# Optimization experiments

Measured on AMD Instinct MI355X. Metric: run time of the kernel, lower is better.

Reference implementation:

```python
import jax, jax.numpy as jnp
import numpy as np

H = 256       # hidden_size
W2V = 300     # word embedding dim
POS = 30      # pos embedding dim
NF = 100      # filters per n-gram CNN
VOCAB = 50000
NPOS = 100
N_EDUS = 1024
L = 20        # tokens per EDU


def setup_inputs() -> dict:
    key = jax.random.key(0)
    ks = jax.random.split(key, 22)
    def nrm(k, shape, s=0.05):
        return jax.random.normal(k, shape, dtype=jnp.float32) * s
    cw = W2V + POS  # CNN input width = 330
    # valid transition sequence: S, then (S, R) repeated n-1 times -> 2n-1 steps
    transes = jnp.concatenate([jnp.zeros((1,), jnp.int32),
                               jnp.tile(jnp.array([0, 1], jnp.int32), N_EDUS - 1)])
    return {
        "edu_words": jax.random.randint(ks[0], (N_EDUS, L), 0, VOCAB),
        "edu_poses": jax.random.randint(ks[1], (N_EDUS, L), 0, NPOS),
        "transes": transes,
        "word_emb": nrm(ks[2], (VOCAB, W2V), 1.0),
        "pos_emb": nrm(ks[3], (NPOS, POS), 1.0),
        "Wu": nrm(ks[4], (NF, 1, 1, cw)), "bu": nrm(ks[5], (NF,)),
        "Wb": nrm(ks[6], (NF, 1, 2, cw)), "bb": nrm(ks[7], (NF,)),
        "Wt": nrm(ks[8], (NF, 1, 3, cw)), "bt": nrm(ks[9], (NF,)),
        "Wp": nrm(ks[10], (2 * H, 2 * W2V + POS + 3 * NF)), "bp": nrm(ks[11], (2 * H,)),
        "Wih": nrm(ks[12], (4 * H, 3 * H)), "Whh": nrm(ks[13], (4 * H, H)),
        "bih": nrm(ks[14], (4 * H,)), "bhh": nrm(ks[15], (4 * H,)),
        "Wc": nrm(ks[16], (5 * H, 3 * H)), "bc": nrm(ks[17], (5 * H,)),
        "Ws": nrm(ks[18], (2, H)), "bs": nrm(ks[19], (2,)),
    }


def _encode_edus(edu_words, edu_poses, word_emb, pos_emb, Wu, bu, Wb, bb, Wt, bt, Wp, bp):
    we = word_emb[edu_words]                # [N, L, 300]
    pe = pos_emb[edu_poses]                 # [N, L, 30]
    x = jnp.concatenate([we, pe], axis=-1)[:, None, :, :]  # NCHW [N,1,L,330]
    def conv_pool(W, b, pad):
        # kernel spans full width -> output width 1; pad only along time
        y = jax.lax.conv_general_dilated(x, W, (1, 1), ((pad, pad), (0, 0)),
                                         dimension_numbers=("NCHW", "OIHW", "NCHW"))[..., 0]
        return jax.nn.relu(y + b[None, :, None]).max(axis=-1)  # [N, F]
    feats = jnp.concatenate([we[:, 0], we[:, -1], pe[:, 0],
                             conv_pool(Wu, bu, 0), conv_pool(Wb, bb, 1),
                             conv_pool(Wt, bt, 2)], axis=-1)   # [N, 930]
    h, c = jnp.split(feats @ Wp.T + bp, 2, axis=-1)
    return h, c


def _parse_loss(edu_words, edu_poses, transes, word_emb, pos_emb, Wu, bu, Wb, bb, Wt, bt,
                Wp, bp, Wih, Whh, bih, bhh, Wc, bc, Ws, bs):
    eh, ec = _encode_edus(edu_words, edu_poses, word_emb, pos_emb, Wu, bu, Wb, bb, Wt, bt, Wp, bp)
    M = N_EDUS + 2
    buf_h = jnp.concatenate([eh, jnp.zeros((2, H), jnp.float32)], axis=0)
    buf_c = jnp.concatenate([ec, jnp.zeros((2, H), jnp.float32)], axis=0)
    stack_h = jnp.zeros((M, H), jnp.float32)  # slots 0,1 are the initial placeholders
    stack_c = jnp.zeros((M, H), jnp.float32)

    def lstm(xv, h, c):  # torch LSTMCell gate order i,f,g,o
        g = xv @ Wih.T + bih + h @ Whh.T + bhh
        i, f, gg, o = jnp.split(g, 4)
        c2 = jax.nn.sigmoid(f) * c + jax.nn.sigmoid(i) * jnp.tanh(gg)
        return jax.nn.sigmoid(o) * jnp.tanh(c2), c2

    def track(sh, sptr, bptr, th, tc):
        xv = jnp.concatenate([sh[sptr - 1], sh[sptr - 2], buf_h[bptr]])
        return lstm(xv, th, tc)

    sptr = jnp.int32(2)
    bptr = jnp.int32(0)
    th, tc = track(stack_h, sptr, bptr, jnp.zeros(H, jnp.float32), jnp.zeros(H, jnp.float32))

    def step(carry, trans):
        sh, sc, sptr, bptr, th, tc = carry
        logits = th @ Ws.T + bs  # scorer MLP with mlp_layers=1 -> single Linear
        is_shift = trans == 0
        # SHIFT candidate: push buffer front
        sh_s = sh.at[sptr].set(buf_h[bptr])
        sc_s = sc.at[sptr].set(buf_c[bptr])
        # REDUCE candidate: tree-LSTM composition of top two stack items
        h1, c1 = sh[sptr - 1], sc[sptr - 1]
        h2, c2 = sh[sptr - 2], sc[sptr - 2]
        g = jnp.concatenate([h1, h2, th]) @ Wc.T + bc
        a, i, f1, f2, o = jnp.split(g, 5)
        rc = jnp.tanh(a) * jax.nn.sigmoid(i) + jax.nn.sigmoid(f1) * c1 + jax.nn.sigmoid(f2) * c2
        rh = jax.nn.sigmoid(o) * jnp.tanh(rc)
        sh_r = sh.at[sptr - 2].set(rh)
        sc_r = sc.at[sptr - 2].set(rc)
        sh2 = jnp.where(is_shift, sh_s, sh_r)
        sc2 = jnp.where(is_shift, sc_s, sc_r)
        sptr2 = jnp.where(is_shift, sptr + 1, sptr - 1)
        bptr2 = jnp.where(is_shift, bptr + 1, bptr)
        th2, tc2 = track(sh2, sptr2, bptr2, th, tc)
        return (sh2, sc2, sptr2, bptr2, th2, tc2), logits

    _, pred = jax.lax.scan(step, (stack_h, stack_c, sptr, bptr, th, tc), transes)
    logp = jax.nn.log_softmax(pred, axis=-1)
    return -jnp.mean(logp[jnp.arange(transes.shape[0]), transes])


def reference(edu_words, edu_poses, transes, word_emb, pos_emb, Wu, bu, Wb, bb, Wt, bt,
              Wp, bp, Wih, Whh, bih, bhh, Wc, bc, Ws, bs):
    return _parse_loss(edu_words, edu_poses, transes, word_emb, pos_emb, Wu, bu, Wb, bb,
                       Wt, bt, Wp, bp, Wih, Whh, bih, bhh, Wc, bc, Ws, bs)
```

## Files before the change

### kernel.cpp

```cpp
#include <hip/hip_runtime.h>
#include <math.h>

#define NEDU  1024
#define LTOK  20
#define CW    330
#define HDIM  256
#define FEAT  930
#define MSLOT 1026
#define NWG   64

#define O_WCATT 0
#define SZ_WCATT (330*600)
#define O_F     (O_WCATT + SZ_WCATT)
#define SZ_F    (NEDU*FEAT)
#define O_BUFH  (O_F + SZ_F)
#define SZ_BUF  (MSLOT*HDIM)
#define O_BUFC  (O_BUFH + SZ_BUF)
#define O_STKT  (O_BUFC + SZ_BUF)
#define O_THT   (O_STKT + MSLOT*HDIM)
#define O_RHT   (O_THT + 2*HDIM)
#define O_LOSSP (O_RHT + HDIM)
#define NZERO   ((MSLOT + 3) * HDIM)

#define AG __HIP_MEMORY_SCOPE_AGENT
__device__ __forceinline__ unsigned long long aload64(const unsigned long long* p) {
  return __hip_atomic_load(p, __ATOMIC_RELAXED, AG);
}
__device__ __forceinline__ void astore(unsigned* p, unsigned v) {
  __hip_atomic_store(p, v, __ATOMIC_RELAXED, AG);
}
__device__ __forceinline__ unsigned tagbits(float v, unsigned ver) {
  return (__float_as_uint(v) & ~3u) | (ver & 3u);
}
__device__ __forceinline__ float sigm(float x) { return 1.f / (1.f + expf(-x)); }

__device__ __forceinline__ void sync_lds() {
  asm volatile("s_waitcnt lgkmcnt(0)\n\ts_barrier" ::: "memory");
}

__device__ __forceinline__ void gather1T(const unsigned* base, int lane, unsigned tag,
                                         float* x) {
  const unsigned long long* p = (const unsigned long long*)base + 2 * lane;
  for (int it = 0;; ++it) {
    const unsigned long long a = aload64(p), b = aload64(p + 1);
    const bool ok = (((unsigned)a & 3u) == tag) & (((unsigned)(a >> 32) & 3u) == tag) &
                    (((unsigned)b & 3u) == tag) & (((unsigned)(b >> 32) & 3u) == tag);
    if (__ballot(ok) == ~0ull) {
      x[0] = __uint_as_float((unsigned)a); x[1] = __uint_as_float((unsigned)(a >> 32));
      x[2] = __uint_as_float((unsigned)b); x[3] = __uint_as_float((unsigned)(b >> 32));
      return;
    }
    if (it > 48) __builtin_amdgcn_s_sleep(1);
  }
}
__device__ __forceinline__ void gather2T(const unsigned* b1, unsigned t1,
                                         const unsigned* b2, unsigned t2,
                                         int lane, float* x1, float* x2) {
  const unsigned long long* p1 = (const unsigned long long*)b1 + 2 * lane;
  const unsigned long long* p2 = (const unsigned long long*)b2 + 2 * lane;
  for (int it = 0;; ++it) {
    const unsigned long long a = aload64(p1), b = aload64(p1 + 1);
    const unsigned long long c = aload64(p2), d = aload64(p2 + 1);
    const bool ok = (((unsigned)a & 3u) == t1) & (((unsigned)(a >> 32) & 3u) == t1) &
                    (((unsigned)b & 3u) == t1) & (((unsigned)(b >> 32) & 3u) == t1) &
                    (((unsigned)c & 3u) == t2) & (((unsigned)(c >> 32) & 3u) == t2) &
                    (((unsigned)d & 3u) == t2) & (((unsigned)(d >> 32) & 3u) == t2);
    if (__ballot(ok) == ~0ull) {
      x1[0] = __uint_as_float((unsigned)a); x1[1] = __uint_as_float((unsigned)(a >> 32));
      x1[2] = __uint_as_float((unsigned)b); x1[3] = __uint_as_float((unsigned)(b >> 32));
      x2[0] = __uint_as_float((unsigned)c); x2[1] = __uint_as_float((unsigned)(c >> 32));
      x2[2] = __uint_as_float((unsigned)d); x2[3] = __uint_as_float((unsigned)(d >> 32));
      return;
    }
    if (it > 48) __builtin_amdgcn_s_sleep(1);
  }
}

__global__ void prep_kernel(const float* __restrict__ Wu, const float* __restrict__ Wb,
                            const float* __restrict__ Wt, float* __restrict__ ws) {
  const int i0 = blockIdx.x * blockDim.x + threadIdx.x;
  const int st = gridDim.x * blockDim.x;
  for (int i = i0; i < SZ_WCATT; i += st) {
    const int k = i / 600, c = i - 600 * k;
    float v;
    if (c < 100)      v = Wu[c * 330 + k];
    else if (c < 300) { const int q = c - 100; v = Wb[(q % 100) * 660 + (q / 100) * 330 + k]; }
    else              { const int q = c - 300; v = Wt[(q % 100) * 990 + (q / 100) * 330 + k]; }
    ws[O_WCATT + i] = v;
  }
  unsigned* z = (unsigned*)ws + O_STKT;
  for (int i = i0; i < NZERO; i += st) z[i] = 0u;
  for (int i = i0; i < 2 * HDIM; i += st) {
    ws[O_BUFH + NEDU * HDIM + i] = 0.f;
    ws[O_BUFC + NEDU * HDIM + i] = 0.f;
  }
}

__global__ __launch_bounds__(256) void encode_kernel(
    const int* __restrict__ edu_words, const int* __restrict__ edu_poses,
    const float* __restrict__ word_emb, const float* __restrict__ pos_emb,
    const float* __restrict__ bu, const float* __restrict__ bb,
    const float* __restrict__ bt, float* __restrict__ ws) {
  __shared__ __align__(16) float xlT[CW * LTOK];
  __shared__ float zl[300 * 21];
  __shared__ float convout[300];
  const int n = blockIdx.x, tid = threadIdx.x;
  const float* WcatT = ws + O_WCATT;

  for (int i = tid; i < LTOK * CW; i += 256) {
    const int l = i / CW, k = i - l * CW;
    float v;
    if (k < 300) v = word_emb[(size_t)edu_words[n * LTOK + l] * 300 + k];
    else         v = pos_emb[(size_t)edu_poses[n * LTOK + l] * 30 + (k - 300)];
    xlT[k * LTOK + l] = v;
  }
  __syncthreads();

  for (int f = tid; f < 300; f += 256) {
    float acc[LTOK];
#pragma unroll
    for (int l = 0; l < LTOK; ++l) acc[l] = 0.f;
    for (int k = 0; k < CW; ++k) {
      const float w = WcatT[k * 600 + f];
      const float4* xp = (const float4*)(xlT + k * LTOK);
      union { float4 v[5]; float s[20]; } xu;
      xu.v[0] = xp[0]; xu.v[1] = xp[1]; xu.v[2] = xp[2]; xu.v[3] = xp[3]; xu.v[4] = xp[4];
#pragma unroll
      for (int l = 0; l < LTOK; ++l) acc[l] += w * xu.s[l];
    }
#pragma unroll
    for (int l = 0; l < LTOK; ++l) zl[f * 21 + l] = acc[l];
  }
  __syncthreads();
  if (tid < 200) {
    float m;
    if (tid < 100) {
      const int f = tid; const float b = bu[f];
      m = zl[f * 21] + b;
      for (int l = 1; l < 20; ++l) m = fmaxf(m, zl[f * 21 + l] + b);
    } else {
      const int f = tid - 100; const float b = bb[f];
      const float* z0 = zl + (100 + f) * 21;
      const float* z1 = zl + (200 + f) * 21;
      m = z1[0] + b;
      for (int u = 1; u <= 19; ++u) m = fmaxf(m, z0[u - 1] + z1[u] + b);
      m = fmaxf(m, z0[19] + b);
    }
    convout[tid] = fmaxf(m, 0.f);
  }
  __syncthreads();

  for (int f = tid; f < 300; f += 256) {
    float acc[LTOK];
#pragma unroll
    for (int l = 0; l < LTOK; ++l) acc[l] = 0.f;
    for (int k = 0; k < CW; ++k) {
      const float w = WcatT[k * 600 + 300 + f];
      const float4* xp = (const float4*)(xlT + k * LTOK);
      union { float4 v[5]; float s[20]; } xu;
      xu.v[0] = xp[0]; xu.v[1] = xp[1]; xu.v[2] = xp[2]; xu.v[3] = xp[3]; xu.v[4] = xp[4];
#pragma unroll
      for (int l = 0; l < LTOK; ++l) acc[l] += w * xu.s[l];
    }
#pragma unroll
    for (int l = 0; l < LTOK; ++l) zl[f * 21 + l] = acc[l];
  }
  __syncthreads();
  if (tid < 100) {
    const int f = tid; const float b = bt[f];
    const float* z0 = zl + f * 21;
    const float* z1 = zl + (100 + f) * 21;
    const float* z2 = zl + (200 + f) * 21;
    float m = z2[0] + b;
    m = fmaxf(m, z1[0] + z2[1] + b);
    for (int u = 2; u <= 19; ++u) m = fmaxf(m, z0[u - 2] + z1[u - 1] + z2[u] + b);
    m = fmaxf(m, z0[18] + z1[19] + b);
    m = fmaxf(m, z0[19] + b);
    convout[200 + f] = fmaxf(m, 0.f);
  }
  __syncthreads();

  float* Fr = ws + O_F + (size_t)n * FEAT;
  for (int j = tid; j < FEAT; j += 256) {
    float v;
    if (j < 300)      v = xlT[j * LTOK + 0];
    else if (j < 600) v = xlT[(j - 300) * LTOK + 19];
    else if (j < 630) v = xlT[(j - 300) * LTOK + 0];
    else              v = convout[j - 630];
    Fr[j] = v;
  }
}

__global__ __launch_bounds__(256) void proj_kernel(const float* __restrict__ Wp,
                                                   const float* __restrict__ bp,
                                                   float* __restrict__ ws) {
  __shared__ float As[64][17];
  __shared__ float Bs[64][17];
  const float* F = ws + O_F;
  float* bufh = ws + O_BUFH;
  float* bufc = ws + O_BUFC;
  const int tid = threadIdx.x;
  const int m0 = blockIdx.x * 64, n0 = blockIdx.y * 64;
  const int mm0 = (tid & 15) * 4, nn0 = (tid >> 4) * 4;
  float acc[4][4] = {{0.f}};
  for (int k0 = 0; k0 < FEAT; k0 += 16) {
    for (int i = tid; i < 64 * 16; i += 256) {
      const int mm = i >> 4, kk = i & 15;
      const int gk = k0 + kk;
      As[mm][kk] = (gk < FEAT) ? F[(size_t)(m0 + mm) * FEAT + gk] : 0.f;
      Bs[mm][kk] = (gk < FEAT) ? Wp[(size_t)(n0 + mm) * FEAT + gk] : 0.f;
    }
    __syncthreads();
#pragma unroll
    for (int kk = 0; kk < 16; ++kk) {
      float av[4], bv[4];
#pragma unroll
      for (int i = 0; i < 4; ++i) av[i] = As[mm0 + i][kk];
#pragma unroll
      for (int j = 0; j < 4; ++j) bv[j] = Bs[nn0 + j][kk];
#pragma unroll
      for (int i = 0; i < 4; ++i)
#pragma unroll
        for (int j = 0; j < 4; ++j) acc[i][j] += av[i] * bv[j];
    }
    __syncthreads();
  }
#pragma unroll
  for (int i = 0; i < 4; ++i) {
    const int m = m0 + mm0 + i;
#pragma unroll
    for (int j = 0; j < 4; ++j) {
      const int nn = n0 + nn0 + j;
      const float v = acc[i][j] + bp[nn];
      if (nn < 256) bufh[(size_t)m * 256 + nn] = v;
      else          bufc[(size_t)m * 256 + (nn - 256)] = v;
    }
  }
}

__global__ __launch_bounds__(256, 1) void parse_kernel(
    const int* __restrict__ transes, int nT,
    const float* __restrict__ Wih, const float* __restrict__ Whh,
    const float* __restrict__ bih, const float* __restrict__ bhh,
    const float* __restrict__ Wc, const float* __restrict__ bc,
    const float* __restrict__ Wsc, float* __restrict__ ws) {
  const int tid = threadIdx.x;
  const int lane = tid & 63;
  const int wv = tid >> 6;
  const int bx = blockIdx.x;
  const int j0 = bx * 4;

  const float* bufh = ws + O_BUFH;
  const float* bufc = ws + O_BUFC;
  unsigned* stkT = (unsigned*)ws + O_STKT;
  unsigned* thT  = (unsigned*)ws + O_THT;
  unsigned* rhT  = (unsigned*)ws + O_RHT;
  float* lossp   = ws + O_LOSSP;

  __shared__ float sc_lds[MSLOT][4];
  __shared__ unsigned vstk[MSLOT];
  __shared__ float tc_lds[2][4];
  __shared__ float g_lds[20];
  __shared__ float rh_st[4];
  __shared__ float part_lds[8];

  float wt[4][16]; float bt_[4];
#pragma unroll
  for (int q = 0; q < 4; ++q) {
    const int rg = wv * 256 + j0 + q;
#pragma unroll
    for (int blk = 0; blk < 3; ++blk) {
      const float4 w = *(const float4*)(Wih + (size_t)rg * 768 + blk * 256 + 4 * lane);
      wt[q][4 * blk + 0] = w.x; wt[q][4 * blk + 1] = w.y;
      wt[q][4 * blk + 2] = w.z; wt[q][4 * blk + 3] = w.w;
    }
    const float4 wh = *(const float4*)(Whh + (size_t)rg * 256 + 4 * lane);
    wt[q][12] = wh.x; wt[q][13] = wh.y; wt[q][14] = wh.z; wt[q][15] = wh.w;
    bt_[q] = bih[rg] + bhh[rg];
  }
  float wcm[5][12]; float bc_[5];
#pragma unroll
  for (int q = 0; q < 5; ++q) {
    const int row = 5 * wv + q, gate = row >> 2, jj = row & 3;
    const int rg = gate * 256 + j0 + jj;
#pragma unroll
    for (int blk = 0; blk < 3; ++blk) {
      const float4 w = *(const float4*)(Wc + (size_t)rg * 768 + blk * 256 + 4 * lane);
      wcm[q][4 * blk + 0] = w.x; wcm[q][4 * blk + 1] = w.y;
      wcm[q][4 * blk + 2] = w.z; wcm[q][4 * blk + 3] = w.w;
    }
    bc_[q] = bc[rg];
  }
  float ws0 = 0.f, ws1 = 0.f;
  if (tid < 4) { ws0 = Wsc[j0 + tid]; ws1 = Wsc[256 + j0 + tid]; }

  for (int i = tid; i < MSLOT; i += 256) vstk[i] = 0u;
  if (tid < 4) { sc_lds[0][tid] = 0.f; sc_lds[1][tid] = 0.f;
                 tc_lds[0][tid] = 0.f; tc_lds[1][tid] = 0.f; }
  __syncthreads();

  unsigned V = 0, vrh = 0;
  int sptr = 2, bptr = 0;

  auto red4 = [&](float& a0, float& a1, float& a2, float& a3) {
#pragma unroll
    for (int off = 32; off; off >>= 1) {
      a0 += __shfl_down(a0, off, 64); a1 += __shfl_down(a1, off, 64);
      a2 += __shfl_down(a2, off, 64); a3 += __shfl_down(a3, off, 64);
    }
  };
  auto red5 = [&](float& a0, float& a1, float& a2, float& a3, float& a4) {
#pragma unroll
    for (int off = 32; off; off >>= 1) {
      a0 += __shfl_down(a0, off, 64); a1 += __shfl_down(a1, off, 64);
      a2 += __shfl_down(a2, off, 64); a3 += __shfl_down(a3, off, 64);
      a4 += __shfl_down(a4, off, 64);
    }
  };

  auto fin_track = [&]() {
    const int j = j0 + tid;
    const float gi = g_lds[tid], gf = g_lds[4 + tid], gg = g_lds[8 + tid], go = g_lds[12 + tid];
    const float cn = sigm(gf) * tc_lds[V & 1][tid] + sigm(gi) * tanhf(gg);
    tc_lds[(V + 1) & 1][tid] = cn;
    const float th = sigm(go) * tanhf(cn);
    astore(thT + ((V + 1) & 1) * HDIM + j, tagbits(th, V + 1));
    part_lds[tid] = ws0 * th; part_lds[4 + tid] = ws1 * th;
  };
  auto emit_loss = [&]() {
    float* lp = lossp + (size_t)V * 128 + bx * 2;
    lp[0] = part_lds[0] + part_lds[1] + part_lds[2] + part_lds[3];
    lp[1] = part_lds[4] + part_lds[5] + part_lds[6] + part_lds[7];
  };
  auto dyn_track = [&](const unsigned* fbase, unsigned ftag, int fblk,
                       float s0, float s1, float s2, float s3) {
    float x[4];
    gather1T(fbase, lane, ftag, x);
    float d0 = 0.f, d1 = 0.f, d2 = 0.f, d3 = 0.f;
#pragma unroll
    for (int c = 0; c < 4; ++c) {
      d0 += wt[0][4 * fblk + c] * x[c]; d1 += wt[1][4 * fblk + c] * x[c];
      d2 += wt[2][4 * fblk + c] * x[c]; d3 += wt[3][4 * fblk + c] * x[c];
    }
    red4(d0, d1, d2, d3);
    if (lane == 0) {
      g_lds[wv * 4 + 0] = s0 + d0 + bt_[0]; g_lds[wv * 4 + 1] = s1 + d1 + bt_[1];
      g_lds[wv * 4 + 2] = s2 + d2 + bt_[2]; g_lds[wv * 4 + 3] = s3 + d3 + bt_[3];
    }
    sync_lds();
    if (tid < 4) fin_track();
    if (tid == 0) emit_loss();
  };

  {
    float p1[4], p2[4];
    gather2T(stkT + HDIM, 0u, stkT, 0u, lane, p1, p2);
    const float4 f3 = *(const float4*)(bufh + 4 * lane);
    const float p3[4] = { f3.x, f3.y, f3.z, f3.w };
    float s0 = 0.f, s1 = 0.f, s2 = 0.f, s3 = 0.f;
#pragma unroll
    for (int c = 0; c < 4; ++c) {
      s0 += wt[0][c] * p1[c] + wt[0][4 + c] * p2[c] + wt[0][8 + c] * p3[c];
      s1 += wt[1][c] * p1[c] + wt[1][4 + c] * p2[c] + wt[1][8 + c] * p3[c];
      s2 += wt[2][c] * p1[c] + wt[2][4 + c] * p2[c] + wt[2][8 + c] * p3[c];
      s3 += wt[3][c] * p1[c] + wt[3][4 + c] * p2[c] + wt[3][8 + c] * p3[c];
    }
    red4(s0, s1, s2, s3);
    dyn_track(thT + (V & 1) * HDIM, V & 3, 3, s0, s1, s2, s3);
    sync_lds();
    V += 1;
  }

  for (int t = 0; t < nT; ++t) {
    const int tr = transes[t];
    if (tr) {
      {
        float h1[4], h2[4];
        gather2T(stkT + (size_t)(sptr - 1) * HDIM, vstk[sptr - 1] & 3,
                 stkT + (size_t)(sptr - 2) * HDIM, vstk[sptr - 2] & 3, lane, h1, h2);
        float s0 = 0.f, s1 = 0.f, s2 = 0.f, s3 = 0.f, s4 = 0.f;
#pragma unroll
        for (int c = 0; c < 4; ++c) {
          s0 += wcm[0][c] * h1[c] + wcm[0][4 + c] * h2[c];
          s1 += wcm[1][c] * h1[c] + wcm[1][4 + c] * h2[c];
          s2 += wcm[2][c] * h1[c] + wcm[2][4 + c] * h2[c];
          s3 += wcm[3][c] * h1[c] + wcm[3][4 + c] * h2[c];
          s4 += wcm[4][c] * h1[c] + wcm[4][4 + c] * h2[c];
        }
        red5(s0, s1, s2, s3, s4);
        float x[4];
        gather1T(thT + (V & 1) * HDIM, lane, V & 3, x);
        float d0 = 0.f, d1 = 0.f, d2 = 0.f, d3 = 0.f, d4 = 0.f;
#pragma unroll
        for (int c = 0; c < 4; ++c) {
          d0 += wcm[0][8 + c] * x[c]; d1 += wcm[1][8 + c] * x[c];
          d2 += wcm[2][8 + c] * x[c]; d3 += wcm[3][8 + c] * x[c];
          d4 += wcm[4][8 + c] * x[c];
        }
        red5(d0, d1, d2, d3, d4);
        if (lane == 0) {
          g_lds[5 * wv + 0] = s0 + d0 + bc_[0]; g_lds[5 * wv + 1] = s1 + d1 + bc_[1];
          g_lds[5 * wv + 2] = s2 + d2 + bc_[2]; g_lds[5 * wv + 3] = s3 + d3 + bc_[3];
          g_lds[5 * wv + 4] = s4 + d4 + bc_[4];
        }
      }
      sync_lds();
      if (tid < 4) {
        const int j = j0 + tid;
        const float ga = g_lds[tid], gi = g_lds[4 + tid], gf1 = g_lds[8 + tid],
                    gf2 = g_lds[12 + tid], go = g_lds[16 + tid];
        const float c1 = sc_lds[sptr - 1][tid];
        const float c2 = sc_lds[sptr - 2][tid];
        const float rc = tanhf(ga) * sigm(gi) + sigm(gf1) * c1 + sigm(gf2) * c2;
        const float rh = sigm(go) * tanhf(rc);
        sc_lds[sptr - 2][tid] = rc;
        rh_st[tid] = rh;
        astore(rhT + j, tagbits(rh, vrh + 1));
      }
      sync_lds();
      vrh += 1;

      {
        const int slot = sptr - 2;
        const unsigned nv = vstk[slot] + 1;
        if (tid < 4)
          astore(stkT + (size_t)slot * HDIM + j0 + tid, tagbits(rh_st[tid], nv));
        float p2[4], xth[4];
        gather2T(stkT + (size_t)(sptr - 3) * HDIM, vstk[sptr - 3] & 3,
                 thT + (V & 1) * HDIM, V & 3, lane, p2, xth);
        const float4 f3 = *(const float4*)(bufh + (size_t)bptr * HDIM + 4 * lane);
        const float p3[4] = { f3.x, f3.y, f3.z, f3.w };
        float s0 = 0.f, s1 = 0.f, s2 = 0.f, s3 = 0.f;
#pragma unroll
        for (int c = 0; c < 4; ++c) {
          s0 += wt[0][4 + c] * p2[c] + wt[0][8 + c] * p3[c] + wt[0][12 + c] * xth[c];
          s1 += wt[1][4 + c] * p2[c] + wt[1][8 + c] * p3[c] + wt[1][12 + c] * xth[c];
          s2 += wt[2][4 + c] * p2[c] + wt[2][8 + c] * p3[c] + wt[2][12 + c] * xth[c];
          s3 += wt[3][4 + c] * p2[c] + wt[3][8 + c] * p3[c] + wt[3][12 + c] * xth[c];
        }
        red4(s0, s1, s2, s3);
        dyn_track(rhT, vrh & 3, 0, s0, s1, s2, s3);
        if (tid == 0) vstk[slot] = nv;
        sync_lds();
        V += 1; sptr -= 1;
      }
    } else {
      const unsigned nv = vstk[sptr] + 1;
      if (tid < 4) {
        const int j = j0 + tid;
        astore(stkT + (size_t)sptr * HDIM + j, tagbits(bufh[(size_t)bptr * HDIM + j], nv));
        sc_lds[sptr][tid] = bufc[(size_t)bptr * HDIM + j];
      }
      const float4 f1 = *(const float4*)(bufh + (size_t)bptr * HDIM + 4 * lane);
      const float4 f3 = *(const float4*)(bufh + (size_t)(bptr + 1) * HDIM + 4 * lane);
      float p2[4];
      gather1T(stkT + (size_t)(sptr - 1) * HDIM, lane, vstk[sptr - 1] & 3, p2);
      const float p1[4] = { f1.x, f1.y, f1.z, f1.w };
      const float p3[4] = { f3.x, f3.y, f3.z, f3.w };
      float s0 = 0.f, s1 = 0.f, s2 = 0.f, s3 = 0.f;
#pragma unroll
      for (int c = 0; c < 4; ++c) {
        s0 += wt[0][c] * p1[c] + wt[0][4 + c] * p2[c] + wt[0][8 + c] * p3[c];
        s1 += wt[1][c] * p1[c] + wt[1][4 + c] * p2[c] + wt[1][8 + c] * p3[c];
        s2 += wt[2][c] * p1[c] + wt[2][4 + c] * p2[c] + wt[2][8 + c] * p3[c];
        s3 += wt[3][c] * p1[c] + wt[3][4 + c] * p2[c] + wt[3][8 + c] * p3[c];
      }
      red4(s0, s1, s2, s3);
      dyn_track(thT + (V & 1) * HDIM, V & 3, 3, s0, s1, s2, s3);
      if (tid == 0) vstk[sptr] = nv;
      sync_lds();
      V += 1; sptr += 1; bptr += 1;
    }
  }
}

__global__ __launch_bounds__(256) void loss_kernel(const int* __restrict__ transes, int nT,
                                                   const float* __restrict__ bsc,
                                                   const float* __restrict__ ws,
                                                   float* __restrict__ out) {
  const int tid = threadIdx.x;
  const float* lossp = ws + O_LOSSP;
  __shared__ double red[256];
  double acc = 0.0;
  for (int t = tid; t < nT; t += 256) {
    const float* lp = lossp + (size_t)t * 128;
    float a0 = 0.f, a1 = 0.f;
    for (int w = 0; w < 64; ++w) { a0 += lp[2 * w]; a1 += lp[2 * w + 1]; }
    const float l0 = a0 + bsc[0], l1 = a1 + bsc[1];
    const float mx = fmaxf(l0, l1);
    acc += (double)(mx + logf(expf(l0 - mx) + expf(l1 - mx)) - (transes[t] ? l1 : l0));
  }
  red[tid] = acc;
  __syncthreads();
  for (int s = 128; s; s >>= 1) {
    if (tid < s) red[tid] += red[tid + s];
    __syncthreads();
  }
  if (tid == 0) out[0] = (float)(red[0] / (double)nT);
}

extern "C" void kernel_launch(void* const* d_in, const int* in_sizes, int n_in,
                              void* d_out, int out_size, void* d_ws, size_t ws_size,
                              hipStream_t stream) {
  const int*   edu_words = (const int*)d_in[0];
  const int*   edu_poses = (const int*)d_in[1];
  const int*   transes   = (const int*)d_in[2];
  const float* word_emb  = (const float*)d_in[3];
  const float* pos_emb   = (const float*)d_in[4];
  const float* Wu  = (const float*)d_in[5];
  const float* bu  = (const float*)d_in[6];
  const float* Wb  = (const float*)d_in[7];
  const float* bb  = (const float*)d_in[8];
  const float* Wt  = (const float*)d_in[9];
  const float* bt  = (const float*)d_in[10];
  const float* Wp  = (const float*)d_in[11];
  const float* bp  = (const float*)d_in[12];
  const float* Wih = (const float*)d_in[13];
  const float* Whh = (const float*)d_in[14];
  const float* bih = (const float*)d_in[15];
  const float* bhh = (const float*)d_in[16];
  const float* Wc  = (const float*)d_in[17];
  const float* bc  = (const float*)d_in[18];
  const float* Wsc = (const float*)d_in[19];
  const float* bsc = (const float*)d_in[20];
  float* ws  = (float*)d_ws;
  float* out = (float*)d_out;
  int nT = in_sizes[2];

  hipLaunchKernelGGL(prep_kernel, dim3(256), dim3(256), 0, stream, Wu, Wb, Wt, ws);
  hipLaunchKernelGGL(encode_kernel, dim3(NEDU), dim3(256), 0, stream,
                     edu_words, edu_poses, word_emb, pos_emb, bu, bb, bt, ws);
  hipLaunchKernelGGL(proj_kernel, dim3(16, 8), dim3(256), 0, stream, Wp, bp, ws);

  void* args[] = { (void*)&transes, (void*)&nT, (void*)&Wih, (void*)&Whh, (void*)&bih,
                   (void*)&bhh, (void*)&Wc, (void*)&bc, (void*)&Wsc, (void*)&ws };
  hipLaunchCooperativeKernel((const void*)parse_kernel, dim3(NWG), dim3(256), args, 0, stream);

  hipLaunchKernelGGL(loss_kernel, dim3(1), dim3(256), 0, stream, transes, nT, bsc, ws, out);
}
```

Measured before the change: 7.783 ms.

## Restructure parse recurrence to one wavefront per hidden unit with double-buffered stack

The parse kernel now runs 256 single-wavefront workgroups, each owning one hidden unit, instead of 64 four-wave workgroups owning four units. All intra-block LDS barriers and shared gate staging are removed, and gate sums are reduced with xor butterflies so every lane holds the result. The stack is double-buffered by version parity so a reduce step's new value can be published and consumed without a separate rh buffer. Tracker-state loads are issued early and polled afterwards to overlap latency. Transitions are cached in LDS and the loss reduction is split into a parallel two-stage kernel. The tradeoff is four times as many cross-workgroup flag polls per step, and the loss-partial buffer now reuses the start of the workspace that the encoder weights occupied.

Result: slower. 13.26 ms (+70.4%).

```diff
diff --git a/kernel.cpp b/kernel.cpp
--- a/kernel.cpp
+++ b/kernel.cpp
@@ -7,23 +7,25 @@
 #define HDIM  256
 #define FEAT  930
 #define MSLOT 1026
-#define NWG   64
 
 #define O_WCATT 0
 #define SZ_WCATT (330*600)
 #define O_F     (O_WCATT + SZ_WCATT)
 #define SZ_F    (NEDU*FEAT)
+#define O_LOSSP 0
+#define SZ_LOSSP (2048*512)
 #define O_BUFH  (O_F + SZ_F)
 #define SZ_BUF  (MSLOT*HDIM)
 #define O_BUFC  (O_BUFH + SZ_BUF)
 #define O_STKT  (O_BUFC + SZ_BUF)
-#define O_THT   (O_STKT + MSLOT*HDIM)
-#define O_RHT   (O_THT + 2*HDIM)
-#define O_LOSSP (O_RHT + HDIM)
-#define NZERO   ((MSLOT + 3) * HDIM)
+#define O_THT   (O_STKT + 2*SZ_BUF)
+#define O_PART  (O_THT + 2*HDIM)
+#define NZERO   ((2*MSLOT + 2) * HDIM)
+
+typedef unsigned long long u64;
 
 #define AG __HIP_MEMORY_SCOPE_AGENT
-__device__ __forceinline__ unsigned long long aload64(const unsigned long long* p) {
+__device__ __forceinline__ u64 aload64(const u64* p) {
   return __hip_atomic_load(p, __ATOMIC_RELAXED, AG);
 }
 __device__ __forceinline__ void astore(unsigned* p, unsigned v) {
@@ -34,15 +36,11 @@
 }
 __device__ __forceinline__ float sigm(float x) { return 1.f / (1.f + expf(-x)); }
 
-__device__ __forceinline__ void sync_lds() {
-  asm volatile("s_waitcnt lgkmcnt(0)\n\ts_barrier" ::: "memory");
-}
-
 __device__ __forceinline__ void gather1T(const unsigned* base, int lane, unsigned tag,
                                          float* x) {
-  const unsigned long long* p = (const unsigned long long*)base + 2 * lane;
+  const u64* p = (const u64*)base + 2 * lane;
   for (int it = 0;; ++it) {
-    const unsigned long long a = aload64(p), b = aload64(p + 1);
+    const u64 a = aload64(p), b = aload64(p + 1);
     const bool ok = (((unsigned)a & 3u) == tag) & (((unsigned)(a >> 32) & 3u) == tag) &
                     (((unsigned)b & 3u) == tag) & (((unsigned)(b >> 32) & 3u) == tag);
     if (__ballot(ok) == ~0ull) {
@@ -56,11 +54,11 @@
 __device__ __forceinline__ void gather2T(const unsigned* b1, unsigned t1,
                                          const unsigned* b2, unsigned t2,
                                          int lane, float* x1, float* x2) {
-  const unsigned long long* p1 = (const unsigned long long*)b1 + 2 * lane;
-  const unsigned long long* p2 = (const unsigned long long*)b2 + 2 * lane;
+  const u64* p1 = (const u64*)b1 + 2 * lane;
+  const u64* p2 = (const u64*)b2 + 2 * lane;
   for (int it = 0;; ++it) {
-    const unsigned long long a = aload64(p1), b = aload64(p1 + 1);
-    const unsigned long long c = aload64(p2), d = aload64(p2 + 1);
+    const u64 a = aload64(p1), b = aload64(p1 + 1);
+    const u64 c = aload64(p2), d = aload64(p2 + 1);
     const bool ok = (((unsigned)a & 3u) == t1) & (((unsigned)(a >> 32) & 3u) == t1) &
                     (((unsigned)b & 3u) == t1) & (((unsigned)(b >> 32) & 3u) == t1) &
                     (((unsigned)c & 3u) == t2) & (((unsigned)(c >> 32) & 3u) == t2) &
@@ -74,6 +72,17 @@
     }
     if (it > 48) __builtin_amdgcn_s_sleep(1);
   }
+}
+__device__ __forceinline__ void spin4(const u64* p, u64 a, u64 b, unsigned tag, float* x) {
+  for (int it = 0;; ++it) {
+    const bool ok = (((unsigned)a & 3u) == tag) & (((unsigned)(a >> 32) & 3u) == tag) &
+                    (((unsigned)b & 3u) == tag) & (((unsigned)(b >> 32) & 3u) == tag);
+    if (__ballot(ok) == ~0ull) break;
+    if (it > 40) __builtin_amdgcn_s_sleep(1);
+    a = aload64(p); b = aload64(p + 1);
+  }
+  x[0] = __uint_as_float((unsigned)a); x[1] = __uint_as_float((unsigned)(a >> 32));
+  x[2] = __uint_as_float((unsigned)b); x[3] = __uint_as_float((unsigned)(b >> 32));
 }
 
 __global__ void prep_kernel(const float* __restrict__ Wu, const float* __restrict__ Wb,
@@ -217,11 +226,11 @@
 #pragma unroll
       for (int i = 0; i < 4; ++i) av[i] = As[mm0 + i][kk];
 #pragma unroll
-      for (int j = 0; j < 4; ++j) bv[j] = Bs[nn0 + j][kk];
+      for (int jj = 0; jj < 4; ++jj) bv[jj] = Bs[nn0 + jj][kk];
 #pragma unroll
       for (int i = 0; i < 4; ++i)
 #pragma unroll
-        for (int j = 0; j < 4; ++j) acc[i][j] += av[i] * bv[j];
+        for (int jj = 0; jj < 4; ++jj) acc[i][jj] += av[i] * bv[jj];
     }
     __syncthreads();
   }
@@ -229,274 +238,255 @@
   for (int i = 0; i < 4; ++i) {
     const int m = m0 + mm0 + i;
 #pragma unroll
-    for (int j = 0; j < 4; ++j) {
-      const int nn = n0 + nn0 + j;
-      const float v = acc[i][j] + bp[nn];
+    for (int jj = 0; jj < 4; ++jj) {
+      const int nn = n0 + nn0 + jj;
+      const float v = acc[i][jj] + bp[nn];
       if (nn < 256) bufh[(size_t)m * 256 + nn] = v;
       else          bufc[(size_t)m * 256 + (nn - 256)] = v;
     }
   }
 }
 
-__global__ __launch_bounds__(256, 1) void parse_kernel(
+__global__ __launch_bounds__(64, 1) void parse_kernel(
     const int* __restrict__ transes, int nT,
     const float* __restrict__ Wih, const float* __restrict__ Whh,
     const float* __restrict__ bih, const float* __restrict__ bhh,
     const float* __restrict__ Wc, const float* __restrict__ bc,
     const float* __restrict__ Wsc, float* __restrict__ ws) {
-  const int tid = threadIdx.x;
-  const int lane = tid & 63;
-  const int wv = tid >> 6;
-  const int bx = blockIdx.x;
-  const int j0 = bx * 4;
+  const int lane = threadIdx.x;
+  const int j = blockIdx.x;
 
   const float* bufh = ws + O_BUFH;
   const float* bufc = ws + O_BUFC;
   unsigned* stkT = (unsigned*)ws + O_STKT;
   unsigned* thT  = (unsigned*)ws + O_THT;
-  unsigned* rhT  = (unsigned*)ws + O_RHT;
   float* lossp   = ws + O_LOSSP;
 
-  __shared__ float sc_lds[MSLOT][4];
   __shared__ unsigned vstk[MSLOT];
-  __shared__ float tc_lds[2][4];
-  __shared__ float g_lds[20];
-  __shared__ float rh_st[4];
-  __shared__ float part_lds[8];
-
-  float wt[4][16]; float bt_[4];
-#pragma unroll
-  for (int q = 0; q < 4; ++q) {
-    const int rg = wv * 256 + j0 + q;
+  __shared__ float    scs[MSLOT];
+  __shared__ int      trs[2048];
+
+  for (int i = lane; i < MSLOT; i += 64) { vstk[i] = 0u; scs[i] = 0.f; }
+  const int nTc = (nT < 2048) ? nT : 2048;
+  for (int i = lane; i < nTc; i += 64) trs[i] = transes[i];
+  __syncthreads();
+
+  float wt[4][16]; float bt4[4];
+#pragma unroll
+  for (int g = 0; g < 4; ++g) {
+    const int rg = g * 256 + j;
 #pragma unroll
     for (int blk = 0; blk < 3; ++blk) {
       const float4 w = *(const float4*)(Wih + (size_t)rg * 768 + blk * 256 + 4 * lane);
-      wt[q][4 * blk + 0] = w.x; wt[q][4 * blk + 1] = w.y;
-      wt[q][4 * blk + 2] = w.z; wt[q][4 * blk + 3] = w.w;
+      wt[g][4 * blk + 0] = w.x; wt[g][4 * blk + 1] = w.y;
+      wt[g][4 * blk + 2] = w.z; wt[g][4 * blk + 3] = w.w;
     }
     const float4 wh = *(const float4*)(Whh + (size_t)rg * 256 + 4 * lane);
-    wt[q][12] = wh.x; wt[q][13] = wh.y; wt[q][14] = wh.z; wt[q][15] = wh.w;
-    bt_[q] = bih[rg] + bhh[rg];
-  }
-  float wcm[5][12]; float bc_[5];
+    wt[g][12] = wh.x; wt[g][13] = wh.y; wt[g][14] = wh.z; wt[g][15] = wh.w;
+    bt4[g] = bih[rg] + bhh[rg];
+  }
+  float wcm[5][12]; float bc5[5];
 #pragma unroll
   for (int q = 0; q < 5; ++q) {
-    const int row = 5 * wv + q, gate = row >> 2, jj = row & 3;
-    const int rg = gate * 256 + j0 + jj;
+    const int rg = q * 256 + j;
 #pragma unroll
     for (int blk = 0; blk < 3; ++blk) {
       const float4 w = *(const float4*)(Wc + (size_t)rg * 768 + blk * 256 + 4 * lane);
       wcm[q][4 * blk + 0] = w.x; wcm[q][4 * blk + 1] = w.y;
       wcm[q][4 * blk + 2] = w.z; wcm[q][4 * blk + 3] = w.w;
     }
-    bc_[q] = bc[rg];
-  }
-  float ws0 = 0.f, ws1 = 0.f;
-  if (tid < 4) { ws0 = Wsc[j0 + tid]; ws1 = Wsc[256 + j0 + tid]; }
-
-  for (int i = tid; i < MSLOT; i += 256) vstk[i] = 0u;
-  if (tid < 4) { sc_lds[0][tid] = 0.f; sc_lds[1][tid] = 0.f;
-                 tc_lds[0][tid] = 0.f; tc_lds[1][tid] = 0.f; }
-  __syncthreads();
-
-  unsigned V = 0, vrh = 0;
+    bc5[q] = bc[rg];
+  }
+  const float ws0 = Wsc[j], ws1 = Wsc[256 + j];
+
+  float tc = 0.f;
+  unsigned V = 0;
   int sptr = 2, bptr = 0;
 
-  auto red4 = [&](float& a0, float& a1, float& a2, float& a3) {
+  auto bfly4 = [&](float& a0, float& a1, float& a2, float& a3) {
 #pragma unroll
     for (int off = 32; off; off >>= 1) {
-      a0 += __shfl_down(a0, off, 64); a1 += __shfl_down(a1, off, 64);
-      a2 += __shfl_down(a2, off, 64); a3 += __shfl_down(a3, off, 64);
+      a0 += __shfl_xor(a0, off, 64); a1 += __shfl_xor(a1, off, 64);
+      a2 += __shfl_xor(a2, off, 64); a3 += __shfl_xor(a3, off, 64);
     }
   };
-  auto red5 = [&](float& a0, float& a1, float& a2, float& a3, float& a4) {
+  auto bfly5 = [&](float& a0, float& a1, float& a2, float& a3, float& a4) {
 #pragma unroll
     for (int off = 32; off; off >>= 1) {
-      a0 += __shfl_down(a0, off, 64); a1 += __shfl_down(a1, off, 64);
-      a2 += __shfl_down(a2, off, 64); a3 += __shfl_down(a3, off, 64);
-      a4 += __shfl_down(a4, off, 64);
+      a0 += __shfl_xor(a0, off, 64); a1 += __shfl_xor(a1, off, 64);
+      a2 += __shfl_xor(a2, off, 64); a3 += __shfl_xor(a3, off, 64);
+      a4 += __shfl_xor(a4, off, 64);
     }
   };
 
-  auto fin_track = [&]() {
-    const int j = j0 + tid;
-    const float gi = g_lds[tid], gf = g_lds[4 + tid], gg = g_lds[8 + tid], go = g_lds[12 + tid];
-    const float cn = sigm(gf) * tc_lds[V & 1][tid] + sigm(gi) * tanhf(gg);
-    tc_lds[(V + 1) & 1][tid] = cn;
+  auto fin_track = [&](float s0, float s1, float s2, float s3) {
+    const float gi = s0 + bt4[0], gf = s1 + bt4[1], gg = s2 + bt4[2], go = s3 + bt4[3];
+    const float cn = sigm(gf) * tc + sigm(gi) * tanhf(gg);
+    tc = cn;
     const float th = sigm(go) * tanhf(cn);
-    astore(thT + ((V + 1) & 1) * HDIM + j, tagbits(th, V + 1));
-    part_lds[tid] = ws0 * th; part_lds[4 + tid] = ws1 * th;
+    if (lane == 0) {
+      astore(thT + ((V + 1) & 1) * HDIM + j, tagbits(th, V + 1));
+      float2 lp; lp.x = ws0 * th; lp.y = ws1 * th;
+      *(float2*)(lossp + (size_t)V * 512 + 2 * j) = lp;
+    }
   };
-  auto emit_loss = [&]() {
-    float* lp = lossp + (size_t)V * 128 + bx * 2;
-    lp[0] = part_lds[0] + part_lds[1] + part_lds[2] + part_lds[3];
-    lp[1] = part_lds[4] + part_lds[5] + part_lds[6] + part_lds[7];
-  };
-  auto dyn_track = [&](const unsigned* fbase, unsigned ftag, int fblk,
-                       float s0, float s1, float s2, float s3) {
-    float x[4];
-    gather1T(fbase, lane, ftag, x);
-    float d0 = 0.f, d1 = 0.f, d2 = 0.f, d3 = 0.f;
+
+  {
+    const float4 f3 = *(const float4*)(bufh + 4 * lane);
+    const float x3[4] = { f3.x, f3.y, f3.z, f3.w };
+    float s0 = 0.f, s1 = 0.f, s2 = 0.f, s3 = 0.f;
 #pragma unroll
     for (int c = 0; c < 4; ++c) {
-      d0 += wt[0][4 * fblk + c] * x[c]; d1 += wt[1][4 * fblk + c] * x[c];
-      d2 += wt[2][4 * fblk + c] * x[c]; d3 += wt[3][4 * fblk + c] * x[c];
-    }
-    red4(d0, d1, d2, d3);
-    if (lane == 0) {
-      g_lds[wv * 4 + 0] = s0 + d0 + bt_[0]; g_lds[wv * 4 + 1] = s1 + d1 + bt_[1];
-      g_lds[wv * 4 + 2] = s2 + d2 + bt_[2]; g_lds[wv * 4 + 3] = s3 + d3 + bt_[3];
-    }
-    sync_lds();
-    if (tid < 4) fin_track();
-    if (tid == 0) emit_loss();
-  };
-
-  {
-    float p1[4], p2[4];
-    gather2T(stkT + HDIM, 0u, stkT, 0u, lane, p1, p2);
-    const float4 f3 = *(const float4*)(bufh + 4 * lane);
-    const float p3[4] = { f3.x, f3.y, f3.z, f3.w };
-    float s0 = 0.f, s1 = 0.f, s2 = 0.f, s3 = 0.f;
-#pragma unroll
-    for (int c = 0; c < 4; ++c) {
-      s0 += wt[0][c] * p1[c] + wt[0][4 + c] * p2[c] + wt[0][8 + c] * p3[c];
-      s1 += wt[1][c] * p1[c] + wt[1][4 + c] * p2[c] + wt[1][8 + c] * p3[c];
-      s2 += wt[2][c] * p1[c] + wt[2][4 + c] * p2[c] + wt[2][8 + c] * p3[c];
-      s3 += wt[3][c] * p1[c] + wt[3][4 + c] * p2[c] + wt[3][8 + c] * p3[c];
-    }
-    red4(s0, s1, s2, s3);
-    dyn_track(thT + (V & 1) * HDIM, V & 3, 3, s0, s1, s2, s3);
-    sync_lds();
-    V += 1;
+      s0 += wt[0][8 + c] * x3[c]; s1 += wt[1][8 + c] * x3[c];
+      s2 += wt[2][8 + c] * x3[c]; s3 += wt[3][8 + c] * x3[c];
+    }
+    bfly4(s0, s1, s2, s3);
+    fin_track(s0, s1, s2, s3);
+    V = 1;
   }
 
   for (int t = 0; t < nT; ++t) {
-    const int tr = transes[t];
+    const int tr = (t < 2048) ? trs[t] : transes[t];
+    const u64* pt = (const u64*)(thT + (V & 1) * HDIM) + 2 * lane;
+    u64 ta = aload64(pt), tb = aload64(pt + 1);
     if (tr) {
-      {
-        float h1[4], h2[4];
-        gather2T(stkT + (size_t)(sptr - 1) * HDIM, vstk[sptr - 1] & 3,
-                 stkT + (size_t)(sptr - 2) * HDIM, vstk[sptr - 2] & 3, lane, h1, h2);
-        float s0 = 0.f, s1 = 0.f, s2 = 0.f, s3 = 0.f, s4 = 0.f;
-#pragma unroll
-        for (int c = 0; c < 4; ++c) {
-          s0 += wcm[0][c] * h1[c] + wcm[0][4 + c] * h2[c];
-          s1 += wcm[1][c] * h1[c] + wcm[1][4 + c] * h2[c];
-          s2 += wcm[2][c] * h1[c] + wcm[2][4 + c] * h2[c];
-          s3 += wcm[3][c] * h1[c] + wcm[3][4 + c] * h2[c];
-          s4 += wcm[4][c] * h1[c] + wcm[4][4 + c] * h2[c];
-        }
-        red5(s0, s1, s2, s3, s4);
-        float x[4];
-        gather1T(thT + (V & 1) * HDIM, lane, V & 3, x);
-        float d0 = 0.f, d1 = 0.f, d2 = 0.f, d3 = 0.f, d4 = 0.f;
-#pragma unroll
-        for (int c = 0; c < 4; ++c) {
-          d0 += wcm[0][8 + c] * x[c]; d1 += wcm[1][8 + c] * x[c];
-          d2 += wcm[2][8 + c] * x[c]; d3 += wcm[3][8 + c] * x[c];
-          d4 += wcm[4][8 + c] * x[c];
-        }
-        red5(d0, d1, d2, d3, d4);
-        if (lane == 0) {
-          g_lds[5 * wv + 0] = s0 + d0 + bc_[0]; g_lds[5 * wv + 1] = s1 + d1 + bc_[1];
-          g_lds[5 * wv + 2] = s2 + d2 + bc_[2]; g_lds[5 * wv + 3] = s3 + d3 + bc_[3];
-          g_lds[5 * wv + 4] = s4 + d4 + bc_[4];
-        }
-      }
-      sync_lds();
-      if (tid < 4) {
-        const int j = j0 + tid;
-        const float ga = g_lds[tid], gi = g_lds[4 + tid], gf1 = g_lds[8 + tid],
-                    gf2 = g_lds[12 + tid], go = g_lds[16 + tid];
-        const float c1 = sc_lds[sptr - 1][tid];
-        const float c2 = sc_lds[sptr - 2][tid];
-        const float rc = tanhf(ga) * sigm(gi) + sigm(gf1) * c1 + sigm(gf2) * c2;
-        const float rh = sigm(go) * tanhf(rc);
-        sc_lds[sptr - 2][tid] = rc;
-        rh_st[tid] = rh;
-        astore(rhT + j, tagbits(rh, vrh + 1));
-      }
-      sync_lds();
-      vrh += 1;
-
-      {
-        const int slot = sptr - 2;
-        const unsigned nv = vstk[slot] + 1;
-        if (tid < 4)
-          astore(stkT + (size_t)slot * HDIM + j0 + tid, tagbits(rh_st[tid], nv));
-        float p2[4], xth[4];
-        gather2T(stkT + (size_t)(sptr - 3) * HDIM, vstk[sptr - 3] & 3,
-                 thT + (V & 1) * HDIM, V & 3, lane, p2, xth);
-        const float4 f3 = *(const float4*)(bufh + (size_t)bptr * HDIM + 4 * lane);
-        const float p3[4] = { f3.x, f3.y, f3.z, f3.w };
-        float s0 = 0.f, s1 = 0.f, s2 = 0.f, s3 = 0.f;
-#pragma unroll
-        for (int c = 0; c < 4; ++c) {
-          s0 += wt[0][4 + c] * p2[c] + wt[0][8 + c] * p3[c] + wt[0][12 + c] * xth[c];
-          s1 += wt[1][4 + c] * p2[c] + wt[1][8 + c] * p3[c] + wt[1][12 + c] * xth[c];
-          s2 += wt[2][4 + c] * p2[c] + wt[2][8 + c] * p3[c] + wt[2][12 + c] * xth[c];
-          s3 += wt[3][4 + c] * p2[c] + wt[3][8 + c] * p3[c] + wt[3][12 + c] * xth[c];
-        }
-        red4(s0, s1, s2, s3);
-        dyn_track(rhT, vrh & 3, 0, s0, s1, s2, s3);
-        if (tid == 0) vstk[slot] = nv;
-        sync_lds();
-        V += 1; sptr -= 1;
-      }
+      const unsigned v1 = vstk[sptr - 1], v2 = vstk[sptr - 2];
+      const unsigned nvr = v2 + 1;
+      const float c1 = scs[sptr - 1], c2 = scs[sptr - 2];
+      float h1[4], h2[4];
+      gather2T(stkT + (size_t)(v1 & 1) * SZ_BUF + (size_t)(sptr - 1) * HDIM, v1 & 3,
+               stkT + (size_t)(v2 & 1) * SZ_BUF + (size_t)(sptr - 2) * HDIM, v2 & 3,
+               lane, h1, h2);
+      float a0 = 0.f, a1 = 0.f, a2 = 0.f, a3 = 0.f, a4 = 0.f;
+#pragma unroll
+      for (int c = 0; c < 4; ++c) {
+        a0 += wcm[0][c] * h1[c] + wcm[0][4 + c] * h2[c];
+        a1 += wcm[1][c] * h1[c] + wcm[1][4 + c] * h2[c];
+        a2 += wcm[2][c] * h1[c] + wcm[2][4 + c] * h2[c];
+        a3 += wcm[3][c] * h1[c] + wcm[3][4 + c] * h2[c];
+        a4 += wcm[4][c] * h1[c] + wcm[4][4 + c] * h2[c];
+      }
+      float xth[4];
+      spin4(pt, ta, tb, V & 3, xth);
+#pragma unroll
+      for (int c = 0; c < 4; ++c) {
+        a0 += wcm[0][8 + c] * xth[c]; a1 += wcm[1][8 + c] * xth[c];
+        a2 += wcm[2][8 + c] * xth[c]; a3 += wcm[3][8 + c] * xth[c];
+        a4 += wcm[4][8 + c] * xth[c];
+      }
+      bfly5(a0, a1, a2, a3, a4);
+      const float rc = tanhf(a0 + bc5[0]) * sigm(a1 + bc5[1])
+                     + sigm(a2 + bc5[2]) * c1 + sigm(a3 + bc5[3]) * c2;
+      const float rh = sigm(a4 + bc5[4]) * tanhf(rc);
+      const int slot = sptr - 2;
+      unsigned* sdst = stkT + (size_t)(nvr & 1) * SZ_BUF + (size_t)slot * HDIM;
+      if (lane == 0) {
+        astore(sdst + j, tagbits(rh, nvr));
+        scs[slot] = rc;
+        vstk[slot] = nvr;
+      }
+      const u64* pr = (const u64*)sdst + 2 * lane;
+      u64 ra = aload64(pr), rb = aload64(pr + 1);
+      const unsigned v3 = vstk[sptr - 3];
+      float p2[4];
+      gather1T(stkT + (size_t)(v3 & 1) * SZ_BUF + (size_t)(sptr - 3) * HDIM, lane,
+               v3 & 3, p2);
+      const float4 f3 = *(const float4*)(bufh + (size_t)bptr * HDIM + 4 * lane);
+      const float x3[4] = { f3.x, f3.y, f3.z, f3.w };
+      float s0 = 0.f, s1 = 0.f, s2 = 0.f, s3 = 0.f;
+#pragma unroll
+      for (int c = 0; c < 4; ++c) {
+        s0 += wt[0][4 + c] * p2[c] + wt[0][8 + c] * x3[c] + wt[0][12 + c] * xth[c];
+        s1 += wt[1][4 + c] * p2[c] + wt[1][8 + c] * x3[c] + wt[1][12 + c] * xth[c];
+        s2 += wt[2][4 + c] * p2[c] + wt[2][8 + c] * x3[c] + wt[2][12 + c] * xth[c];
+        s3 += wt[3][4 + c] * p2[c] + wt[3][8 + c] * x3[c] + wt[3][12 + c] * xth[c];
+      }
+      float rr[4];
+      spin4(pr, ra, rb, nvr & 3, rr);
+#pragma unroll
+      for (int c = 0; c < 4; ++c) {
+        s0 += wt[0][c] * rr[c]; s1 += wt[1][c] * rr[c];
+        s2 += wt[2][c] * rr[c]; s3 += wt[3][c] * rr[c];
+      }
+      bfly4(s0, s1, s2, s3);
+      fin_track(s0, s1, s2, s3);
+      V += 1; sptr -= 1;
     } else {
+      const unsigned v1 = vstk[sptr - 1];
       const unsigned nv = vstk[sptr] + 1;
-      if (tid < 4) {
-        const int j = j0 + tid;
-        astore(stkT + (size_t)sptr * HDIM + j, tagbits(bufh[(size_t)bptr * HDIM + j], nv));
-        sc_lds[sptr][tid] = bufc[(size_t)bptr * HDIM + j];
-      }
       const float4 f1 = *(const float4*)(bufh + (size_t)bptr * HDIM + 4 * lane);
       const float4 f3 = *(const float4*)(bufh + (size_t)(bptr + 1) * HDIM + 4 * lane);
+      if (lane == 0) {
+        astore(stkT + (size_t)(nv & 1) * SZ_BUF + (size_t)sptr * HDIM + j,
+               tagbits(bufh[(size_t)bptr * HDIM + j], nv));
+        scs[sptr] = bufc[(size_t)bptr * HDIM + j];
+        vstk[sptr] = nv;
+      }
       float p2[4];
-      gather1T(stkT + (size_t)(sptr - 1) * HDIM, lane, vstk[sptr - 1] & 3, p2);
-      const float p1[4] = { f1.x, f1.y, f1.z, f1.w };
-      const float p3[4] = { f3.x, f3.y, f3.z, f3.w };
+      gather1T(stkT + (size_t)(v1 & 1) * SZ_BUF + (size_t)(sptr - 1) * HDIM, lane,
+               v1 & 3, p2);
+      const float x1[4] = { f1.x, f1.y, f1.z, f1.w };
+      const float x3[4] = { f3.x, f3.y, f3.z, f3.w };
       float s0 = 0.f, s1 = 0.f, s2 = 0.f, s3 = 0.f;
 #pragma unroll
       for (int c = 0; c < 4; ++c) {
-        s0 += wt[0][c] * p1[c] + wt[0][4 + c] * p2[c] + wt[0][8 + c] * p3[c];
-        s1 += wt[1][c] * p1[c] + wt[1][4 + c] * p2[c] + wt[1][8 + c] * p3[c];
-        s2 += wt[2][c] * p1[c] + wt[2][4 + c] * p2[c] + wt[2][8 + c] * p3[c];
-        s3 += wt[3][c] * p1[c] + wt[3][4 + c] * p2[c] + wt[3][8 + c] * p3[c];
-      }
-      red4(s0, s1, s2, s3);
-      dyn_track(thT + (V & 1) * HDIM, V & 3, 3, s0, s1, s2, s3);
-      if (tid == 0) vstk[sptr] = nv;
-      sync_lds();
+        s0 += wt[0][c] * x1[c] + wt[0][4 + c] * p2[c] + wt[0][8 + c] * x3[c];
+        s1 += wt[1][c] * x1[c] + wt[1][4 + c] * p2[c] + wt[1][8 + c] * x3[c];
+        s2 += wt[2][c] * x1[c] + wt[2][4 + c] * p2[c] + wt[2][8 + c] * x3[c];
+        s3 += wt[3][c] * x1[c] + wt[3][4 + c] * p2[c] + wt[3][8 + c] * x3[c];
+      }
+      float xth[4];
+      spin4(pt, ta, tb, V & 3, xth);
+#pragma unroll
+      for (int c = 0; c < 4; ++c) {
+        s0 += wt[0][12 + c] * xth[c]; s1 += wt[1][12 + c] * xth[c];
+        s2 += wt[2][12 + c] * xth[c]; s3 += wt[3][12 + c] * xth[c];
+      }
+      bfly4(s0, s1, s2, s3);
+      fin_track(s0, s1, s2, s3);
       V += 1; sptr += 1; bptr += 1;
     }
   }
 }
 
-__global__ __launch_bounds__(256) void loss_kernel(const int* __restrict__ transes, int nT,
-                                                   const float* __restrict__ bsc,
-                                                   const float* __restrict__ ws,
-                                                   float* __restrict__ out) {
+__global__ __launch_bounds__(256) void loss1_kernel(const int* __restrict__ transes, int nT,
+                                                    const float* __restrict__ bsc,
+                                                    const float* __restrict__ ws,
+                                                    double* __restrict__ part) {
   const int tid = threadIdx.x;
   const float* lossp = ws + O_LOSSP;
-  __shared__ double red[256];
+  __shared__ float r0s[4], r1s[4];
+  const float b0 = bsc[0], b1 = bsc[1];
   double acc = 0.0;
-  for (int t = tid; t < nT; t += 256) {
-    const float* lp = lossp + (size_t)t * 128;
-    float a0 = 0.f, a1 = 0.f;
-    for (int w = 0; w < 64; ++w) { a0 += lp[2 * w]; a1 += lp[2 * w + 1]; }
-    const float l0 = a0 + bsc[0], l1 = a1 + bsc[1];
-    const float mx = fmaxf(l0, l1);
-    acc += (double)(mx + logf(expf(l0 - mx) + expf(l1 - mx)) - (transes[t] ? l1 : l0));
-  }
-  red[tid] = acc;
-  __syncthreads();
-  for (int s = 128; s; s >>= 1) {
-    if (tid < s) red[tid] += red[tid + s];
+  const int t0 = blockIdx.x * 32;
+  const int t1 = (t0 + 32 < nT) ? t0 + 32 : nT;
+  for (int t = t0; t < t1; ++t) {
+    const float2 p = *(const float2*)(lossp + (size_t)t * 512 + 2 * tid);
+    float a0 = p.x, a1 = p.y;
+#pragma unroll
+    for (int off = 32; off; off >>= 1) {
+      a0 += __shfl_down(a0, off, 64);
+      a1 += __shfl_down(a1, off, 64);
+    }
+    if ((tid & 63) == 0) { r0s[tid >> 6] = a0; r1s[tid >> 6] = a1; }
     __syncthreads();
-  }
-  if (tid == 0) out[0] = (float)(red[0] / (double)nT);
+    if (tid == 0) {
+      const float l0 = r0s[0] + r0s[1] + r0s[2] + r0s[3] + b0;
+      const float l1 = r1s[0] + r1s[1] + r1s[2] + r1s[3] + b1;
+      const float mx = fmaxf(l0, l1);
+      acc += (double)(mx + logf(expf(l0 - mx) + expf(l1 - mx)) - (transes[t] ? l1 : l0));
+    }
+    __syncthreads();
+  }
+  if (tid == 0) part[blockIdx.x] = acc;
+}
+
+__global__ __launch_bounds__(64) void loss2_kernel(int nT, const double* __restrict__ part,
+                                                   float* __restrict__ out) {
+  double a = part[threadIdx.x];
+#pragma unroll
+  for (int off = 32; off; off >>= 1) a += __shfl_down(a, off, 64);
+  if (threadIdx.x == 0) out[0] = (float)(a / (double)nT);
 }
 
 extern "C" void kernel_launch(void* const* d_in, const int* in_sizes, int n_in,
@@ -534,7 +524,11 @@
 
   void* args[] = { (void*)&transes, (void*)&nT, (void*)&Wih, (void*)&Whh, (void*)&bih,
                    (void*)&bhh, (void*)&Wc, (void*)&bc, (void*)&Wsc, (void*)&ws };
-  hipLaunchCooperativeKernel((const void*)parse_kernel, dim3(NWG), dim3(256), args, 0, stream);
-
-  hipLaunchKernelGGL(loss_kernel, dim3(1), dim3(256), 0, stream, transes, nT, bsc, ws, out);
-}
+  hipLaunchCooperativeKernel((const void*)parse_kernel, dim3(256), dim3(64), args, 0, stream);
+
+  double* part = (double*)(ws + O_PART);
+  hipLaunchKernelGGL(loss1_kernel, dim3(64), dim3(256), 0, stream, transes, nT, bsc,
+                     (const float*)ws, part);
+  hipLaunchKernelGGL(loss2_kernel, dim3(1), dim3(64), 0, stream, nT,
+                     (const double*)part, out);
+}
```
